# Kernel tuning notes

Hardware: AMD Instinct MI355X
Metric: run time of the kernel (lower is better)

The kernel has to match this reference:

```python
import jax, jax.numpy as jnp
import numpy as np

B, S, D = 4, 2048, 1024
H = 16
HD = D // H

def setup_inputs() -> dict:
    key = jax.random.key(0)
    ks = jax.random.split(key, 6)
    s = 0.02
    return {
        "input_tensor": jax.random.normal(ks[0], (B, S, D), dtype=jnp.float32),
        "Wq": jax.random.normal(ks[1], (D, D), dtype=jnp.float32) * s,
        "Wk": jax.random.normal(ks[2], (D, D), dtype=jnp.float32) * s,
        "Wv": jax.random.normal(ks[3], (D, D), dtype=jnp.float32) * s,
        "Wo": jax.random.normal(ks[4], (D, D), dtype=jnp.float32) * s,
        "bo": jax.random.normal(ks[5], (D,), dtype=jnp.float32) * s,
    }

def reference(input_tensor, Wq, Wk, Wv, Wo, bo):
    b, n, _ = input_tensor.shape
    # projections (nn.Linear: x @ W.T; bias=False for qkv)
    q = jnp.einsum('bnd,ed->bne', input_tensor, Wq).reshape(b, n, H, HD).transpose(0, 2, 1, 3)
    k = jnp.einsum('bnd,ed->bne', input_tensor, Wk).reshape(b, n, H, HD).transpose(0, 2, 1, 3)
    v = jnp.einsum('bnd,ed->bne', input_tensor, Wv).reshape(b, n, H, HD).transpose(0, 2, 1, 3)
    scores = jnp.einsum('bhqd,bhkd->bhqk', q, k)  # [B,H,S,S]
    causal = jnp.triu(jnp.ones((n, n), dtype=bool), k=1)
    scores = jnp.where(causal, -jnp.inf, scores)
    weights = jax.nn.softmax(scores / jnp.sqrt(jnp.float32(HD)), axis=-1)
    ctx = jnp.einsum('bhqk,bhkd->bhqd', weights, v)  # [B,H,S,HD]
    ctx = ctx.transpose(0, 2, 1, 3).reshape(b, n, D)
    return jnp.einsum('bnd,ed->bne', ctx, Wo) + bo
```

## Files before the change

kernel.cpp:

```cpp
#include <hip/hip_runtime.h>
#include <stdint.h>

#define S_LEN 2048
#define DIM   1024
#define NH    16
#define HD    64
#define BATCH 4
#define M_ROWS (BATCH * S_LEN)

typedef __attribute__((ext_vector_type(8))) __bf16 bf16x8;
typedef __attribute__((ext_vector_type(4))) float  f32x4;

union Frag { bf16x8 v; uint4 q; };

__device__ __forceinline__ ushort f2bf(float f) {
  union { float f; unsigned u; } x; x.f = f;
  unsigned r = x.u + 0x7fffu + ((x.u >> 16) & 1u);
  return (ushort)(r >> 16);
}
__device__ __forceinline__ ushort f2bf_n(float f) {
  union { __bf16 b; ushort u; } x; x.b = (__bf16)f; return x.u;
}

__device__ __forceinline__ f32x4 mfma16(const Frag& a, const Frag& b, f32x4 c) {
  return __builtin_amdgcn_mfma_f32_16x16x32_bf16(a.v, b.v, c, 0, 0, 0);
}

__device__ __forceinline__ void gld_lds16(const ushort* g, ushort* l) {
  __builtin_amdgcn_global_load_lds(
      (__attribute__((address_space(1))) void*)g,
      (__attribute__((address_space(3))) void*)l, 16, 0, 0);
}

__global__ void cast_x_kernel(const float* __restrict__ src, ushort* __restrict__ dst) {
  int i = blockIdx.x * 256 + threadIdx.x;
  float4 f = ((const float4*)src)[i];
  ushort4 u; u.x = f2bf(f.x); u.y = f2bf(f.y); u.z = f2bf(f.z); u.w = f2bf(f.w);
  ((ushort4*)dst)[i] = u;
}

__global__ void cast_w_kernel(const float* __restrict__ w0, const float* __restrict__ w1,
                              const float* __restrict__ w2, const float* __restrict__ w3,
                              ushort* __restrict__ d0, ushort* __restrict__ d1,
                              ushort* __restrict__ d2, ushort* __restrict__ d3) {
  const float* s; ushort* d;
  int z = blockIdx.y;
  if (z == 0) { s = w0; d = d0; } else if (z == 1) { s = w1; d = d1; }
  else if (z == 2) { s = w2; d = d2; } else { s = w3; d = d3; }
  int i = blockIdx.x * 256 + threadIdx.x;
  float4 f = ((const float4*)s)[i];
  ushort4 u; u.x = f2bf(f.x); u.y = f2bf(f.y); u.z = f2bf(f.z); u.w = f2bf(f.w);
  ((ushort4*)d)[i] = u;
}

template <int MODE>
__global__ __launch_bounds__(256)
void gemm_bk64(const ushort* __restrict__ A,
               const ushort* __restrict__ B0, const ushort* __restrict__ B1,
               const ushort* __restrict__ B2,
               ushort* __restrict__ Qb, ushort* __restrict__ Kb, ushort* __restrict__ Vtb,
               float* __restrict__ outf, const float* __restrict__ bias, float scaleq) {
  __shared__ __align__(16) ushort As[128 * 64];
  __shared__ __align__(16) ushort Bs[128 * 64];
  const int K = DIM;
  int lane = threadIdx.x & 63, wave = threadIdx.x >> 6;
  int quad = lane >> 4, l15 = lane & 15;
  int rowBase = blockIdx.y * 128;
  int wsel, colBase;
  const ushort* Bt;
  if (MODE == 0) {
    wsel = blockIdx.x >> 3;
    colBase = (blockIdx.x & 7) * 128;
    Bt = (wsel == 0) ? B0 : (wsel == 1) ? B1 : B2;
  } else {
    wsel = 0;
    colBase = blockIdx.x * 128;
    Bt = B0;
  }
  int wm = (wave >> 1) * 64, wn = (wave & 1) * 64;

  const ushort* Ag = A + (size_t)rowBase * K;
  const ushort* Bg = Bt + (size_t)colBase * K;

  f32x4 acc[4][4];
#pragma unroll
  for (int i = 0; i < 4; i++)
#pragma unroll
    for (int j = 0; j < 4; j++) acc[i][j] = (f32x4){0.f, 0.f, 0.f, 0.f};

  for (int k0 = 0; k0 < K; k0 += 64) {
#pragma unroll
    for (int cc = 0; cc < 4; ++cc) {
      int c = wave * 4 + cc;
      int s = c * 64 + lane;
      int row = s >> 3;
      int c8 = (s & 7) ^ (row & 7);
      gld_lds16(Ag + (size_t)row * K + k0 + c8 * 8, &As[c * 512]);
      gld_lds16(Bg + (size_t)row * K + k0 + c8 * 8, &Bs[c * 512]);
    }
    __syncthreads();
    Frag af[4][2], bf[4][2];
#pragma unroll
    for (int t = 0; t < 4; t++) {
      int ar = wm + t * 16 + l15;
      int br = wn + t * 16 + l15;
#pragma unroll
      for (int kk = 0; kk < 2; kk++) {
        af[t][kk].q = *(const uint4*)&As[ar * 64 + (((kk * 4 + quad) ^ (ar & 7))) * 8];
        bf[t][kk].q = *(const uint4*)&Bs[br * 64 + (((kk * 4 + quad) ^ (br & 7))) * 8];
      }
    }
#pragma unroll
    for (int kk = 0; kk < 2; kk++)
#pragma unroll
      for (int i = 0; i < 4; i++)
#pragma unroll
        for (int j = 0; j < 4; j++) acc[i][j] = mfma16(af[i][kk], bf[j][kk], acc[i][j]);
    __syncthreads();
  }

#pragma unroll
  for (int i = 0; i < 4; i++) {
    int rowt = wm + i * 16 + quad * 4;
#pragma unroll
    for (int j = 0; j < 4; j++) {
      int e = colBase + wn + j * 16 + l15;
      if (MODE == 0) {
        int h = e >> 6, hd = e & 63;
        if (wsel < 2) {
          ushort* dst = wsel ? Kb : Qb;
          float sc = wsel ? 1.f : scaleq;
#pragma unroll
          for (int r = 0; r < 4; r++) {
            int m = rowBase + rowt + r;
            int b = m >> 11, s = m & (S_LEN - 1);
            dst[((size_t)((b * NH + h) * S_LEN + s) << 6) + hd] = f2bf(acc[i][j][r] * sc);
          }
        } else {
          int m0 = rowBase + rowt;
          int b = m0 >> 11, s0 = m0 & (S_LEN - 1);
          ushort4 u;
          u.x = f2bf(acc[i][j][0]); u.y = f2bf(acc[i][j][1]);
          u.z = f2bf(acc[i][j][2]); u.w = f2bf(acc[i][j][3]);
          *(ushort4*)&Vtb[((size_t)((b * NH + h) * HD + hd) << 11) + s0] = u;
        }
      } else {
        float bv = bias[e];
#pragma unroll
        for (int r = 0; r < 4; r++) {
          int m = rowBase + rowt + r;
          outf[(size_t)m * DIM + e] = acc[i][j][r] + bv;
        }
      }
    }
  }
}

__global__ __launch_bounds__(256)
void flash_attn(const ushort* __restrict__ Qb, const ushort* __restrict__ Kb,
                const ushort* __restrict__ Vtb, ushort* __restrict__ Ctx) {
  __shared__ __align__(16) ushort Ks[128 * 64];
  __shared__ __align__(16) ushort Vs[64 * 128];

  int lane = threadIdx.x & 63, wave = threadIdx.x >> 6;
  int quad = lane >> 4, l15 = lane & 15;
  int bh = blockIdx.x;
  int yq = blockIdx.y >> 2, yr = blockIdx.y & 3;
  int qt = (yq == 0) ? (15 - yr) : (yq == 1) ? (8 + yr) : (yq == 2) ? (4 + yr) : (3 - yr);
  int q0 = qt * 128, wq0 = wave * 32;

  const ushort* Qh = Qb + (size_t)bh * S_LEN * HD;
  const ushort* Kh = Kb + (size_t)bh * S_LEN * HD;
  const ushort* Vh = Vtb + (size_t)bh * HD * S_LEN;

#pragma unroll
  for (int cc = 0; cc < 4; ++cc) {
    int c = wave * 4 + cc;
    int s = c * 64 + lane;
    int row = s >> 3;
    int c8 = (s & 7) ^ (row & 7);
    gld_lds16(Qh + (size_t)(q0 + row) * HD + c8 * 8, &Ks[c * 512]);
  }
  __syncthreads();
  Frag qf[2][2];
#pragma unroll
  for (int it = 0; it < 2; ++it)
#pragma unroll
    for (int ks = 0; ks < 2; ++ks) {
      int row = wq0 + it * 16 + l15;
      int c8 = (ks * 4 + quad) ^ (row & 7);
      qf[it][ks].q = *(const uint4*)&Ks[row * 64 + c8 * 8];
    }
  __syncthreads();

  Frag onesf;
  onesf.q = (uint4){0x3F803F80u, 0x3F803F80u, 0x3F803F80u, 0x3F803F80u};

  f32x4 lacc[2];
  f32x4 oacc[2][4];
#pragma unroll
  for (int it = 0; it < 2; ++it) {
    lacc[it] = (f32x4){0.f, 0.f, 0.f, 0.f};
#pragma unroll
    for (int dt = 0; dt < 4; ++dt) oacc[it][dt] = (f32x4){0.f, 0.f, 0.f, 0.f};
  }

  for (int kt = 0; kt <= qt; ++kt) {
#pragma unroll
    for (int cc = 0; cc < 4; ++cc) {
      int c = wave * 4 + cc;
      int s = c * 64 + lane;
      int krow = s >> 3, kc8 = (s & 7) ^ (krow & 7);
      int vrow = s >> 4, vc8 = (s & 15) ^ (vrow & 15);
      gld_lds16(Kh + (size_t)(kt * 128 + krow) * HD + kc8 * 8, &Ks[c * 512]);
      gld_lds16(Vh + (size_t)vrow * S_LEN + kt * 128 + vc8 * 8, &Vs[c * 512]);
    }
    __syncthreads();

    f32x4 sacc[2][8];
    __builtin_amdgcn_s_setprio(1);
#pragma unroll
    for (int jt = 0; jt < 8; ++jt) {
      int row = jt * 16 + l15;
      Frag kf0, kf1;
      kf0.q = *(const uint4*)&Ks[row * 64 + ((quad ^ (row & 7))) * 8];
      kf1.q = *(const uint4*)&Ks[row * 64 + (((4 + quad) ^ (row & 7))) * 8];
#pragma unroll
      for (int it = 0; it < 2; ++it) {
        f32x4 a = (f32x4){0.f, 0.f, 0.f, 0.f};
        a = mfma16(kf0, qf[it][0], a);
        a = mfma16(kf1, qf[it][1], a);
        sacc[it][jt] = a;
      }
    }
    __builtin_amdgcn_s_setprio(0);

    if (kt == qt) {
#pragma unroll
      for (int it = 0; it < 2; ++it)
#pragma unroll
        for (int jt = 0; jt < 8; ++jt)
#pragma unroll
          for (int r = 0; r < 4; ++r)
            if (jt * 16 + quad * 4 + r > wq0 + it * 16 + l15)
              sacc[it][jt][r] = -1e30f;
    }

    uint sw[2][8][2];
#pragma unroll
    for (int it = 0; it < 2; ++it)
#pragma unroll
      for (int jt = 0; jt < 8; ++jt) {
        float p0 = exp2f(sacc[it][jt][0]);
        float p1 = exp2f(sacc[it][jt][1]);
        float p2 = exp2f(sacc[it][jt][2]);
        float p3 = exp2f(sacc[it][jt][3]);
        union { ushort2 h; uint u; } w0, w1;
        w0.h.x = f2bf_n(p0); w0.h.y = f2bf_n(p1);
        w1.h.x = f2bf_n(p2); w1.h.y = f2bf_n(p3);
        sw[it][jt][0] = w0.u;
        sw[it][jt][1] = w1.u;
      }

    Frag pf[2][4];
#pragma unroll
    for (int it = 0; it < 2; ++it)
#pragma unroll
      for (int ks = 0; ks < 4; ++ks) {
        uint x0 = sw[it][2 * ks][0], y0 = sw[it][2 * ks + 1][0];
        uint x1 = sw[it][2 * ks][1], y1 = sw[it][2 * ks + 1][1];
        asm("v_permlane32_swap_b32 %0, %1" : "+v"(x0), "+v"(y0));
        asm("v_permlane16_swap_b32 %0, %1" : "+v"(x0), "+v"(y0));
        asm("v_permlane32_swap_b32 %0, %1" : "+v"(x1), "+v"(y1));
        asm("v_permlane16_swap_b32 %0, %1" : "+v"(x1), "+v"(y1));
        pf[it][ks].q = (uint4){x0, x1, y0, y1};
      }

    __builtin_amdgcn_s_setprio(1);
#pragma unroll
    for (int dt = 0; dt < 4; ++dt) {
      int row = dt * 16 + l15;
      Frag vf[4];
#pragma unroll
      for (int ks = 0; ks < 4; ++ks)
        vf[ks].q = *(const uint4*)&Vs[row * 128 + (((ks * 4 + quad) ^ (row & 15))) * 8];
#pragma unroll
      for (int it = 0; it < 2; ++it) {
        f32x4 a = oacc[it][dt];
#pragma unroll
        for (int ks = 0; ks < 4; ++ks) a = mfma16(pf[it][ks], vf[ks], a);
        oacc[it][dt] = a;
      }
    }
#pragma unroll
    for (int it = 0; it < 2; ++it) {
      f32x4 a = lacc[it];
#pragma unroll
      for (int ks = 0; ks < 4; ++ks) a = mfma16(pf[it][ks], onesf, a);
      lacc[it] = a;
    }
    __builtin_amdgcn_s_setprio(0);

    __syncthreads();
  }

  int b = bh >> 4, h = bh & 15;
#pragma unroll
  for (int it = 0; it < 2; ++it) {
    float lr[4];
#pragma unroll
    for (int r = 0; r < 4; ++r) lr[r] = 1.f / lacc[it][r];
#pragma unroll
    for (int r = 0; r < 4; ++r) {
      int qg = q0 + wq0 + it * 16 + quad * 4 + r;
      size_t base = ((size_t)(b * S_LEN + qg)) * DIM + h * HD;
#pragma unroll
      for (int dt = 0; dt < 4; ++dt)
        Ctx[base + dt * 16 + l15] = f2bf_n(oacc[it][dt][r] * lr[r]);
    }
  }
}

extern "C" void kernel_launch(void* const* d_in, const int* in_sizes, int n_in,
                              void* d_out, int out_size, void* d_ws, size_t ws_size,
                              hipStream_t stream) {
  (void)in_sizes; (void)n_in; (void)out_size; (void)ws_size;
  const float* x  = (const float*)d_in[0];
  const float* Wq = (const float*)d_in[1];
  const float* Wk = (const float*)d_in[2];
  const float* Wv = (const float*)d_in[3];
  const float* Wo = (const float*)d_in[4];
  const float* bo = (const float*)d_in[5];
  float* out = (float*)d_out;

  ushort* Xb  = (ushort*)d_ws;
  ushort* Wqb = Xb  + (size_t)M_ROWS * DIM;
  ushort* Wkb = Wqb + (size_t)DIM * DIM;
  ushort* Wvb = Wkb + (size_t)DIM * DIM;
  ushort* Wob = Wvb + (size_t)DIM * DIM;
  ushort* Qb  = Wob + (size_t)DIM * DIM;
  ushort* Kb  = Qb  + (size_t)M_ROWS * DIM;
  ushort* Vtb = Kb  + (size_t)M_ROWS * DIM;
  ushort* Ctx = Vtb + (size_t)M_ROWS * DIM;

  const float SCALE_Q = 0.18033688011112042f;

  cast_x_kernel<<<dim3(M_ROWS * DIM / 1024), 256, 0, stream>>>(x, Xb);
  cast_w_kernel<<<dim3(DIM * DIM / 1024, 4), 256, 0, stream>>>(Wq, Wk, Wv, Wo, Wqb, Wkb, Wvb, Wob);

  gemm_bk64<0><<<dim3(24, 64), 256, 0, stream>>>(Xb, Wqb, Wkb, Wvb, Qb, Kb, Vtb,
                                                 nullptr, nullptr, SCALE_Q);

  flash_attn<<<dim3(BATCH * NH, S_LEN / 128), 256, 0, stream>>>(Qb, Kb, Vtb, Ctx);

  gemm_bk64<1><<<dim3(8, 64), 256, 0, stream>>>(Ctx, Wob, nullptr, nullptr, nullptr, nullptr,
                                                nullptr, out, bo, 1.0f);
}
```

Before: 263.3 us.

## Pair complementary causal query tiles per block to share K/V loads

Each flash-attention block now processes two query tiles (15-p and p), so every block does the same amount of causal work, and K/V tiles loaded into shared memory are reused for both tiles while the lower one is still active. The grid shrinks from 16 to 8 blocks along y. This removes the causal load imbalance and roughly halves redundant K/V global loads for the paired tiles. In exchange it doubles the accumulator and Q-fragment register footprint, which may lower occupancy, and with 512 blocks total there is less parallelism to fill the GPU.

Measured after the change: 280.8 us. 6.6% more time.

```diff
diff --git a/kernel.cpp b/kernel.cpp
--- a/kernel.cpp
+++ b/kernel.cpp
@@ -165,9 +165,9 @@
   int lane = threadIdx.x & 63, wave = threadIdx.x >> 6;
   int quad = lane >> 4, l15 = lane & 15;
   int bh = blockIdx.x;
-  int yq = blockIdx.y >> 2, yr = blockIdx.y & 3;
-  int qt = (yq == 0) ? (15 - yr) : (yq == 1) ? (8 + yr) : (yq == 2) ? (4 + yr) : (3 - yr);
-  int q0 = qt * 128, wq0 = wave * 32;
+  int pr = blockIdx.y;
+  int qtA = 15 - pr, qtB = pr;
+  int q0A = qtA * 128, q0B = qtB * 128, wq0 = wave * 32;
 
   const ushort* Qh = Qb + (size_t)bh * S_LEN * HD;
   const ushort* Kh = Kb + (size_t)bh * S_LEN * HD;
@@ -179,44 +179,40 @@
     int s = c * 64 + lane;
     int row = s >> 3;
     int c8 = (s & 7) ^ (row & 7);
-    gld_lds16(Qh + (size_t)(q0 + row) * HD + c8 * 8, &Ks[c * 512]);
+    gld_lds16(Qh + (size_t)(q0A + row) * HD + c8 * 8, &Ks[c * 512]);
+    gld_lds16(Qh + (size_t)(q0B + row) * HD + c8 * 8, &Vs[c * 512]);
   }
   __syncthreads();
-  Frag qf[2][2];
+  Frag qfA[2][2], qfB[2][2];
 #pragma unroll
   for (int it = 0; it < 2; ++it)
 #pragma unroll
     for (int ks = 0; ks < 2; ++ks) {
       int row = wq0 + it * 16 + l15;
       int c8 = (ks * 4 + quad) ^ (row & 7);
-      qf[it][ks].q = *(const uint4*)&Ks[row * 64 + c8 * 8];
+      qfA[it][ks].q = *(const uint4*)&Ks[row * 64 + c8 * 8];
+      qfB[it][ks].q = *(const uint4*)&Vs[row * 64 + c8 * 8];
     }
   __syncthreads();
 
   Frag onesf;
   onesf.q = (uint4){0x3F803F80u, 0x3F803F80u, 0x3F803F80u, 0x3F803F80u};
 
-  f32x4 lacc[2];
-  f32x4 oacc[2][4];
+  f32x4 laccA[2], laccB[2];
+  f32x4 oaccA[2][4], oaccB[2][4];
 #pragma unroll
   for (int it = 0; it < 2; ++it) {
-    lacc[it] = (f32x4){0.f, 0.f, 0.f, 0.f};
-#pragma unroll
-    for (int dt = 0; dt < 4; ++dt) oacc[it][dt] = (f32x4){0.f, 0.f, 0.f, 0.f};
-  }
-
-  for (int kt = 0; kt <= qt; ++kt) {
-#pragma unroll
-    for (int cc = 0; cc < 4; ++cc) {
-      int c = wave * 4 + cc;
-      int s = c * 64 + lane;
-      int krow = s >> 3, kc8 = (s & 7) ^ (krow & 7);
-      int vrow = s >> 4, vc8 = (s & 15) ^ (vrow & 15);
-      gld_lds16(Kh + (size_t)(kt * 128 + krow) * HD + kc8 * 8, &Ks[c * 512]);
-      gld_lds16(Vh + (size_t)vrow * S_LEN + kt * 128 + vc8 * 8, &Vs[c * 512]);
-    }
-    __syncthreads();
-
+    laccA[it] = (f32x4){0.f, 0.f, 0.f, 0.f};
+    laccB[it] = (f32x4){0.f, 0.f, 0.f, 0.f};
+#pragma unroll
+    for (int dt = 0; dt < 4; ++dt) {
+      oaccA[it][dt] = (f32x4){0.f, 0.f, 0.f, 0.f};
+      oaccB[it][dt] = (f32x4){0.f, 0.f, 0.f, 0.f};
+    }
+  }
+
+  auto attn_tile = [&](const Frag (&qf)[2][2], f32x4 (&oacc)[2][4],
+                       f32x4 (&lacc)[2], bool diag) {
     f32x4 sacc[2][8];
     __builtin_amdgcn_s_setprio(1);
 #pragma unroll
@@ -235,7 +231,7 @@
     }
     __builtin_amdgcn_s_setprio(0);
 
-    if (kt == qt) {
+    if (diag) {
 #pragma unroll
       for (int it = 0; it < 2; ++it)
 #pragma unroll
@@ -300,25 +296,45 @@
       lacc[it] = a;
     }
     __builtin_amdgcn_s_setprio(0);
-
+  };
+
+  for (int kt = 0; kt <= qtA; ++kt) {
+#pragma unroll
+    for (int cc = 0; cc < 4; ++cc) {
+      int c = wave * 4 + cc;
+      int s = c * 64 + lane;
+      int krow = s >> 3, kc8 = (s & 7) ^ (krow & 7);
+      int vrow = s >> 4, vc8 = (s & 15) ^ (vrow & 15);
+      gld_lds16(Kh + (size_t)(kt * 128 + krow) * HD + kc8 * 8, &Ks[c * 512]);
+      gld_lds16(Vh + (size_t)vrow * S_LEN + kt * 128 + vc8 * 8, &Vs[c * 512]);
+    }
     __syncthreads();
+
+    attn_tile(qfA, oaccA, laccA, kt == qtA);
+    if (kt <= qtB) attn_tile(qfB, oaccB, laccB, kt == qtB);
+
+    __syncthreads();
   }
 
   int b = bh >> 4, h = bh & 15;
-#pragma unroll
-  for (int it = 0; it < 2; ++it) {
-    float lr[4];
-#pragma unroll
-    for (int r = 0; r < 4; ++r) lr[r] = 1.f / lacc[it][r];
-#pragma unroll
-    for (int r = 0; r < 4; ++r) {
-      int qg = q0 + wq0 + it * 16 + quad * 4 + r;
-      size_t base = ((size_t)(b * S_LEN + qg)) * DIM + h * HD;
-#pragma unroll
-      for (int dt = 0; dt < 4; ++dt)
-        Ctx[base + dt * 16 + l15] = f2bf_n(oacc[it][dt][r] * lr[r]);
-    }
-  }
+  auto store_tile = [&](int q0, f32x4 (&oacc)[2][4], f32x4 (&lacc)[2]) {
+#pragma unroll
+    for (int it = 0; it < 2; ++it) {
+      float lr[4];
+#pragma unroll
+      for (int r = 0; r < 4; ++r) lr[r] = 1.f / lacc[it][r];
+#pragma unroll
+      for (int r = 0; r < 4; ++r) {
+        int qg = q0 + wq0 + it * 16 + quad * 4 + r;
+        size_t base = ((size_t)(b * S_LEN + qg)) * DIM + h * HD;
+#pragma unroll
+        for (int dt = 0; dt < 4; ++dt)
+          Ctx[base + dt * 16 + l15] = f2bf_n(oacc[it][dt][r] * lr[r]);
+      }
+    }
+  };
+  store_tile(q0A, oaccA, laccA);
+  store_tile(q0B, oaccB, laccB);
 }
 
 extern "C" void kernel_launch(void* const* d_in, const int* in_sizes, int n_in,
@@ -351,7 +367,7 @@
   gemm_bk64<0><<<dim3(24, 64), 256, 0, stream>>>(Xb, Wqb, Wkb, Wvb, Qb, Kb, Vtb,
                                                  nullptr, nullptr, SCALE_Q);
 
-  flash_attn<<<dim3(BATCH * NH, S_LEN / 128), 256, 0, stream>>>(Qb, Kb, Vtb, Ctx);
+  flash_attn<<<dim3(BATCH * NH, 8), 256, 0, stream>>>(Qb, Kb, Vtb, Ctx);
 
   gemm_bk64<1><<<dim3(8, 64), 256, 0, stream>>>(Ctx, Wob, nullptr, nullptr, nullptr, nullptr,
                                                 nullptr, out, bo, 1.0f);
```
